# Kernel optimization log

Measured on AMD Instinct MI355X. Metric: run time of the kernel, lower is better.

## Reference

```python
import jax, jax.numpy as jnp
import numpy as np

N_CHARS, EMB, HID = 256, 512, 2048
HIN = EMB + HID  # concat(input_embedding, hidden)
SEQ_LEN = 4096


def setup_inputs() -> dict:
    key = jax.random.key(0)
    ks = jax.random.split(key, 8)
    w = lambda k, shape: (jax.random.normal(k, shape, jnp.float32) / np.sqrt(shape[-1])).astype(jnp.float32)
    return {
        "input_seq": jax.random.randint(ks[0], (SEQ_LEN,), 0, N_CHARS),
        "emb": jax.random.normal(ks[1], (N_CHARS, EMB), jnp.float32) * 0.02,
        "Wf": w(ks[2], (HID, HIN)), "bf": jnp.zeros((HID,), jnp.float32),
        "Wi": w(ks[3], (HID, HIN)), "bi": jnp.zeros((HID,), jnp.float32),
        "Wo": w(ks[4], (HID, HIN)), "bo": jnp.zeros((HID,), jnp.float32),
        "Wc": w(ks[5], (HID, HIN)), "bc": jnp.zeros((HID,), jnp.float32),
        "Wout": w(ks[6], (N_CHARS, HID)), "bout": jnp.zeros((N_CHARS,), jnp.float32),
    }


def reference(input_seq, emb, Wf, bf, Wi, bi, Wo, bo, Wc, bc, Wout, bout):
    x = emb[input_seq]  # [T, EMB]
    H = Wf.shape[0]

    def step(carry, xt):
        h, c = carry
        hi = jnp.concatenate([xt, h])               # [EMB+HID]
        f = jax.nn.sigmoid(Wf @ hi + bf)            # forget gate
        i = jax.nn.sigmoid(Wi @ hi + bi)            # input gate
        o = jax.nn.sigmoid(Wo @ hi + bo)            # output gate
        g = jnp.tanh(Wc @ hi + bc)                  # cell candidate
        c_new = f * c + i * g
        h_new = o * jnp.tanh(c_new)
        out = Wout @ h_new + bout                   # [N_CHARS]
        return (h_new, c_new), out

    init = (jnp.zeros((H,), x.dtype), jnp.zeros((H,), x.dtype))
    (h_last, c_last), out_seq = jax.lax.scan(step, init, x)
    return out_seq, h_last, c_last
```

## Files before the change

kernel.cpp:

```cpp
#include <hip/hip_runtime.h>

#define NCU     256
#define TPB     512
#define HID     2048
#define EMBD    512
#define HIN     2560
#define TSTEPS  4096
#define NCH     256

typedef unsigned long long u64;
typedef float f32x4 __attribute__((ext_vector_type(4)));

__device__ __forceinline__ float sig_(float x) { return 1.f / (1.f + __expf(-x)); }
__device__ __forceinline__ float th_(float x)  { float e = __expf(2.f * x); return 1.f - 2.f / (e + 1.f); }

__device__ __forceinline__ u64 ld_slot(const u64* p) {
    return __hip_atomic_load(p, __ATOMIC_RELAXED, __HIP_MEMORY_SCOPE_AGENT);
}

__device__ __forceinline__ float dot4(f32x4 a, f32x4 b) {
    return a.x * b.x + a.y * b.y + a.z * b.z + a.w * b.w;
}

#define PIN(v) asm volatile("" : "+v"(v))

extern "C" __global__ void __launch_bounds__(TPB, 2)
lstm_persist(const int* __restrict__ seq,
             const float* __restrict__ emb,
             const float* __restrict__ Wf, const float* __restrict__ bf,
             const float* __restrict__ Wi, const float* __restrict__ bi,
             const float* __restrict__ Wo, const float* __restrict__ bo,
             const float* __restrict__ Wc, const float* __restrict__ bc,
             const float* __restrict__ Wout, const float* __restrict__ bout,
             float* __restrict__ dout,
             u64* __restrict__ hbuf)
{
    const int b    = blockIdx.x;
    const int tid  = threadIdx.x;
    const int wave = tid >> 6;
    const int lane = tid & 63;
    const int hidx = b * 8 + wave;

    __shared__ float hs[HID];
    __shared__ float wpart[8];

    f32x4 wh[4][8], wx[4][2], wr;
    {
        const float* Wm[4] = { Wf, Wi, Wo, Wc };
        #pragma unroll
        for (int g = 0; g < 4; ++g) {
            const float* base = Wm[g] + (size_t)hidx * HIN;
            #pragma unroll
            for (int j = 0; j < 8; ++j)
                wh[g][j] = *(const f32x4*)(base + EMBD + 4 * lane + 256 * j);
            #pragma unroll
            for (int j = 0; j < 2; ++j)
                wx[g][j] = *(const f32x4*)(base + 4 * lane + 256 * j);
        }
        wr = *(const f32x4*)(Wout + (size_t)b * HID + 4 * tid);
    }
    const float bias0 = bf[hidx], bias1 = bi[hidx], bias2 = bo[hidx], bias3 = bc[hidx];
    const float boutb = bout[b];

    float c = 0.f;
    int ch = seq[0];

    for (int t = 0; t <= TSTEPS; ++t) {
        #pragma unroll
        for (int g = 0; g < 4; ++g) {
            #pragma unroll
            for (int j = 0; j < 8; ++j) PIN(wh[g][j]);
            PIN(wx[g][0]); PIN(wx[g][1]);
        }
        PIN(wr);

        float a0 = bias0, a1 = bias1, a2 = bias2, a3 = bias3;
        if (t < TSTEPS) {
            const float* erow = emb + (size_t)ch * EMBD;
            const f32x4 xv0 = *(const f32x4*)(erow + 4 * lane);
            const f32x4 xv1 = *(const f32x4*)(erow + 4 * lane + 256);
            a0 += dot4(wx[0][0], xv0) + dot4(wx[0][1], xv1);
            a1 += dot4(wx[1][0], xv0) + dot4(wx[1][1], xv1);
            a2 += dot4(wx[2][0], xv0) + dot4(wx[2][1], xv1);
            a3 += dot4(wx[3][0], xv0) + dot4(wx[3][1], xv1);
        }
        const int ch_next = (t + 1 < TSTEPS) ? seq[t + 1] : 0;

        if (t == 0) {
            #pragma unroll
            for (int k = 0; k < 4; ++k) hs[tid + 512 * k] = 0.f;
        } else {
            const u64* src = hbuf + (size_t)(t & 1) * HID;
            const u64* p0 = src + tid;
            const u64* p1 = src + tid + 512;
            const u64* p2 = src + tid + 1024;
            const u64* p3 = src + tid + 1536;
            const unsigned tt = (unsigned)t;
            u64 v0 = ld_slot(p0), v1 = ld_slot(p1), v2 = ld_slot(p2), v3 = ld_slot(p3);
            while (((unsigned)(v0 >> 32) != tt) | ((unsigned)(v1 >> 32) != tt) |
                   ((unsigned)(v2 >> 32) != tt) | ((unsigned)(v3 >> 32) != tt)) {
                __builtin_amdgcn_s_sleep(1);
                v0 = ld_slot(p0); v1 = ld_slot(p1); v2 = ld_slot(p2); v3 = ld_slot(p3);
            }
            hs[tid]        = __uint_as_float((unsigned)v0);
            hs[tid + 512]  = __uint_as_float((unsigned)v1);
            hs[tid + 1024] = __uint_as_float((unsigned)v2);
            hs[tid + 1536] = __uint_as_float((unsigned)v3);
        }
        __syncthreads();

        if (t < TSTEPS) {
            #pragma unroll
            for (int j = 0; j < 8; ++j) {
                const f32x4 hv = *(const f32x4*)&hs[4 * lane + 256 * j];
                a0 += dot4(wh[0][j], hv);
                a1 += dot4(wh[1][j], hv);
                a2 += dot4(wh[2][j], hv);
                a3 += dot4(wh[3][j], hv);
            }
            #pragma unroll
            for (int m = 32; m >= 1; m >>= 1) {
                a0 += __shfl_xor(a0, m, 64);
                a1 += __shfl_xor(a1, m, 64);
                a2 += __shfl_xor(a2, m, 64);
                a3 += __shfl_xor(a3, m, 64);
            }
            const float f = sig_(a0);
            const float i = sig_(a1);
            const float o = sig_(a2);
            const float g = th_(a3);
            c = f * c + i * g;
            const float hn = o * th_(c);
            if (lane == 0) {
                const u64 pk = ((u64)(unsigned)(t + 1) << 32) | (u64)__float_as_uint(hn);
                __hip_atomic_store(hbuf + (size_t)((t + 1) & 1) * HID + hidx, pk,
                                   __ATOMIC_RELAXED, __HIP_MEMORY_SCOPE_AGENT);
                if (t == TSTEPS - 1) {
                    dout[(size_t)TSTEPS * NCH + hidx]       = hn;
                    dout[(size_t)TSTEPS * NCH + HID + hidx] = c;
                }
            }
        }

        if (t > 0) {
            const f32x4 hv = *(const f32x4*)&hs[4 * tid];
            float op = dot4(wr, hv);
            #pragma unroll
            for (int m = 32; m >= 1; m >>= 1) op += __shfl_xor(op, m, 64);
            if (lane == 0) wpart[wave] = op;
        }
        __syncthreads();

        if (tid == 0 && t > 0) {
            float s = wpart[0] + wpart[1] + wpart[2] + wpart[3]
                    + wpart[4] + wpart[5] + wpart[6] + wpart[7];
            dout[(size_t)(t - 1) * NCH + b] = s + boutb;
        }
        ch = ch_next;
    }
}

extern "C" void kernel_launch(void* const* d_in, const int* in_sizes, int n_in,
                              void* d_out, int out_size, void* d_ws, size_t ws_size,
                              hipStream_t stream) {
    const int*   seq  = (const int*)d_in[0];
    const float* emb  = (const float*)d_in[1];
    const float* Wf   = (const float*)d_in[2];
    const float* bf   = (const float*)d_in[3];
    const float* Wi   = (const float*)d_in[4];
    const float* bi   = (const float*)d_in[5];
    const float* Wo   = (const float*)d_in[6];
    const float* bo   = (const float*)d_in[7];
    const float* Wc   = (const float*)d_in[8];
    const float* bc   = (const float*)d_in[9];
    const float* Wout = (const float*)d_in[10];
    const float* bout = (const float*)d_in[11];
    float* dout = (float*)d_out;
    u64*   hbuf = (u64*)d_ws;

    hipMemsetAsync(d_ws, 0, 2 * HID * sizeof(u64), stream);
    hipLaunchKernelGGL(lstm_persist, dim3(NCU), dim3(TPB), 0, stream,
                       seq, emb, Wf, bf, Wi, bi, Wo, bo, Wc, bc, Wout, bout,
                       dout, hbuf);
}
```

Measured before the change: 10.34 ms.

## Halve block size and map two hidden rows per wave using half-waves

Reduces the block from 8 waves to 4, with each half-wave (32 lanes) owning one hidden row, so every thread holds twice as many register-resident weights. Reductions shrink to a 5-step shuffle and the barrier involves fewer waves, cutting the per-step synchronisation and polling traffic. In exchange, register pressure roughly doubles per thread (about 160 f32x4 vectors), which risks spills. Each step also does more serial FMA work per thread, and each thread now polls 8 slots instead of 4.

```diff
diff --git a/kernel.cpp b/kernel.cpp
--- a/kernel.cpp
+++ b/kernel.cpp
@@ -1,7 +1,7 @@
 #include <hip/hip_runtime.h>
 
 #define NCU     256
-#define TPB     512
+#define TPB     256
 #define HID     2048
 #define EMBD    512
 #define HIN     2560
@@ -24,7 +24,7 @@
 
 #define PIN(v) asm volatile("" : "+v"(v))
 
-extern "C" __global__ void __launch_bounds__(TPB, 2)
+extern "C" __global__ void __launch_bounds__(TPB, 1)
 lstm_persist(const int* __restrict__ seq,
              const float* __restrict__ emb,
              const float* __restrict__ Wf, const float* __restrict__ bf,
@@ -39,27 +39,39 @@
     const int tid  = threadIdx.x;
     const int wave = tid >> 6;
     const int lane = tid & 63;
-    const int hidx = b * 8 + wave;
+    const int half = lane >> 5;
+    const int s    = lane & 31;
+    const int R    = b * 8 + 2 * wave + half;
 
     __shared__ float hs[HID];
-    __shared__ float wpart[8];
-
-    f32x4 wh[4][8], wx[4][2], wr;
+    __shared__ float wpart[4];
+
+    f32x4 wh0[16], wh1[16], wh2[16], wh3[16];
+    f32x4 wx0[4],  wx1[4],  wx2[4],  wx3[4];
+    f32x4 wr0, wr1;
     {
-        const float* Wm[4] = { Wf, Wi, Wo, Wc };
-        #pragma unroll
-        for (int g = 0; g < 4; ++g) {
-            const float* base = Wm[g] + (size_t)hidx * HIN;
-            #pragma unroll
-            for (int j = 0; j < 8; ++j)
-                wh[g][j] = *(const f32x4*)(base + EMBD + 4 * lane + 256 * j);
-            #pragma unroll
-            for (int j = 0; j < 2; ++j)
-                wx[g][j] = *(const f32x4*)(base + 4 * lane + 256 * j);
-        }
-        wr = *(const f32x4*)(Wout + (size_t)b * HID + 4 * tid);
+        const float* b0 = Wf + (size_t)R * HIN;
+        const float* b1 = Wi + (size_t)R * HIN;
+        const float* b2 = Wo + (size_t)R * HIN;
+        const float* b3 = Wc + (size_t)R * HIN;
+        #pragma unroll
+        for (int j = 0; j < 16; ++j) {
+            wh0[j] = *(const f32x4*)(b0 + EMBD + 4 * s + 128 * j);
+            wh1[j] = *(const f32x4*)(b1 + EMBD + 4 * s + 128 * j);
+            wh2[j] = *(const f32x4*)(b2 + EMBD + 4 * s + 128 * j);
+            wh3[j] = *(const f32x4*)(b3 + EMBD + 4 * s + 128 * j);
+        }
+        #pragma unroll
+        for (int j = 0; j < 4; ++j) {
+            wx0[j] = *(const f32x4*)(b0 + 4 * s + 128 * j);
+            wx1[j] = *(const f32x4*)(b1 + 4 * s + 128 * j);
+            wx2[j] = *(const f32x4*)(b2 + 4 * s + 128 * j);
+            wx3[j] = *(const f32x4*)(b3 + 4 * s + 128 * j);
+        }
+        wr0 = *(const f32x4*)(Wout + (size_t)b * HID + 8 * tid);
+        wr1 = *(const f32x4*)(Wout + (size_t)b * HID + 8 * tid + 4);
     }
-    const float bias0 = bf[hidx], bias1 = bi[hidx], bias2 = bo[hidx], bias3 = bc[hidx];
+    const float bias0 = bf[R], bias1 = bi[R], bias2 = bo[R], bias3 = bc[R];
     const float boutb = bout[b];
 
     float c = 0.f;
@@ -67,59 +79,71 @@
 
     for (int t = 0; t <= TSTEPS; ++t) {
         #pragma unroll
-        for (int g = 0; g < 4; ++g) {
-            #pragma unroll
-            for (int j = 0; j < 8; ++j) PIN(wh[g][j]);
-            PIN(wx[g][0]); PIN(wx[g][1]);
-        }
-        PIN(wr);
+        for (int j = 0; j < 16; ++j) { PIN(wh0[j]); PIN(wh1[j]); PIN(wh2[j]); PIN(wh3[j]); }
+        #pragma unroll
+        for (int j = 0; j < 4; ++j)  { PIN(wx0[j]); PIN(wx1[j]); PIN(wx2[j]); PIN(wx3[j]); }
+        PIN(wr0); PIN(wr1);
 
         float a0 = bias0, a1 = bias1, a2 = bias2, a3 = bias3;
         if (t < TSTEPS) {
             const float* erow = emb + (size_t)ch * EMBD;
-            const f32x4 xv0 = *(const f32x4*)(erow + 4 * lane);
-            const f32x4 xv1 = *(const f32x4*)(erow + 4 * lane + 256);
-            a0 += dot4(wx[0][0], xv0) + dot4(wx[0][1], xv1);
-            a1 += dot4(wx[1][0], xv0) + dot4(wx[1][1], xv1);
-            a2 += dot4(wx[2][0], xv0) + dot4(wx[2][1], xv1);
-            a3 += dot4(wx[3][0], xv0) + dot4(wx[3][1], xv1);
+            #pragma unroll
+            for (int j = 0; j < 4; ++j) {
+                const f32x4 xv = *(const f32x4*)(erow + 4 * s + 128 * j);
+                a0 += dot4(wx0[j], xv);
+                a1 += dot4(wx1[j], xv);
+                a2 += dot4(wx2[j], xv);
+                a3 += dot4(wx3[j], xv);
+            }
         }
         const int ch_next = (t + 1 < TSTEPS) ? seq[t + 1] : 0;
 
         if (t == 0) {
             #pragma unroll
-            for (int k = 0; k < 4; ++k) hs[tid + 512 * k] = 0.f;
+            for (int k = 0; k < 8; ++k) hs[tid + 256 * k] = 0.f;
         } else {
             const u64* src = hbuf + (size_t)(t & 1) * HID;
-            const u64* p0 = src + tid;
-            const u64* p1 = src + tid + 512;
-            const u64* p2 = src + tid + 1024;
-            const u64* p3 = src + tid + 1536;
             const unsigned tt = (unsigned)t;
-            u64 v0 = ld_slot(p0), v1 = ld_slot(p1), v2 = ld_slot(p2), v3 = ld_slot(p3);
+            u64 v0 = ld_slot(src + tid);
+            u64 v1 = ld_slot(src + tid + 256);
+            u64 v2 = ld_slot(src + tid + 512);
+            u64 v3 = ld_slot(src + tid + 768);
+            u64 v4 = ld_slot(src + tid + 1024);
+            u64 v5 = ld_slot(src + tid + 1280);
+            u64 v6 = ld_slot(src + tid + 1536);
+            u64 v7 = ld_slot(src + tid + 1792);
             while (((unsigned)(v0 >> 32) != tt) | ((unsigned)(v1 >> 32) != tt) |
-                   ((unsigned)(v2 >> 32) != tt) | ((unsigned)(v3 >> 32) != tt)) {
+                   ((unsigned)(v2 >> 32) != tt) | ((unsigned)(v3 >> 32) != tt) |
+                   ((unsigned)(v4 >> 32) != tt) | ((unsigned)(v5 >> 32) != tt) |
+                   ((unsigned)(v6 >> 32) != tt) | ((unsigned)(v7 >> 32) != tt)) {
                 __builtin_amdgcn_s_sleep(1);
-                v0 = ld_slot(p0); v1 = ld_slot(p1); v2 = ld_slot(p2); v3 = ld_slot(p3);
+                v0 = ld_slot(src + tid);        v1 = ld_slot(src + tid + 256);
+                v2 = ld_slot(src + tid + 512);  v3 = ld_slot(src + tid + 768);
+                v4 = ld_slot(src + tid + 1024); v5 = ld_slot(src + tid + 1280);
+                v6 = ld_slot(src + tid + 1536); v7 = ld_slot(src + tid + 1792);
             }
             hs[tid]        = __uint_as_float((unsigned)v0);
-            hs[tid + 512]  = __uint_as_float((unsigned)v1);
-            hs[tid + 1024] = __uint_as_float((unsigned)v2);
-            hs[tid + 1536] = __uint_as_float((unsigned)v3);
+            hs[tid + 256]  = __uint_as_float((unsigned)v1);
+            hs[tid + 512]  = __uint_as_float((unsigned)v2);
+            hs[tid + 768]  = __uint_as_float((unsigned)v3);
+            hs[tid + 1024] = __uint_as_float((unsigned)v4);
+            hs[tid + 1280] = __uint_as_float((unsigned)v5);
+            hs[tid + 1536] = __uint_as_float((unsigned)v6);
+            hs[tid + 1792] = __uint_as_float((unsigned)v7);
         }
         __syncthreads();
 
         if (t < TSTEPS) {
             #pragma unroll
-            for (int j = 0; j < 8; ++j) {
-                const f32x4 hv = *(const f32x4*)&hs[4 * lane + 256 * j];
-                a0 += dot4(wh[0][j], hv);
-                a1 += dot4(wh[1][j], hv);
-                a2 += dot4(wh[2][j], hv);
-                a3 += dot4(wh[3][j], hv);
-            }
-            #pragma unroll
-            for (int m = 32; m >= 1; m >>= 1) {
+            for (int j = 0; j < 16; ++j) {
+                const f32x4 hv = *(const f32x4*)&hs[4 * s + 128 * j];
+                a0 += dot4(wh0[j], hv);
+                a1 += dot4(wh1[j], hv);
+                a2 += dot4(wh2[j], hv);
+                a3 += dot4(wh3[j], hv);
+            }
+            #pragma unroll
+            for (int m = 16; m >= 1; m >>= 1) {
                 a0 += __shfl_xor(a0, m, 64);
                 a1 += __shfl_xor(a1, m, 64);
                 a2 += __shfl_xor(a2, m, 64);
@@ -131,20 +155,21 @@
             const float g = th_(a3);
             c = f * c + i * g;
             const float hn = o * th_(c);
-            if (lane == 0) {
+            if (s == 0) {
                 const u64 pk = ((u64)(unsigned)(t + 1) << 32) | (u64)__float_as_uint(hn);
-                __hip_atomic_store(hbuf + (size_t)((t + 1) & 1) * HID + hidx, pk,
+                __hip_atomic_store(hbuf + (size_t)((t + 1) & 1) * HID + R, pk,
                                    __ATOMIC_RELAXED, __HIP_MEMORY_SCOPE_AGENT);
                 if (t == TSTEPS - 1) {
-                    dout[(size_t)TSTEPS * NCH + hidx]       = hn;
-                    dout[(size_t)TSTEPS * NCH + HID + hidx] = c;
+                    dout[(size_t)TSTEPS * NCH + R]       = hn;
+                    dout[(size_t)TSTEPS * NCH + HID + R] = c;
                 }
             }
         }
 
         if (t > 0) {
-            const f32x4 hv = *(const f32x4*)&hs[4 * tid];
-            float op = dot4(wr, hv);
+            const f32x4 h0 = *(const f32x4*)&hs[8 * tid];
+            const f32x4 h1 = *(const f32x4*)&hs[8 * tid + 4];
+            float op = dot4(wr0, h0) + dot4(wr1, h1);
             #pragma unroll
             for (int m = 32; m >= 1; m >>= 1) op += __shfl_xor(op, m, 64);
             if (lane == 0) wpart[wave] = op;
@@ -152,9 +177,8 @@
         __syncthreads();
 
         if (tid == 0 && t > 0) {
-            float s = wpart[0] + wpart[1] + wpart[2] + wpart[3]
-                    + wpart[4] + wpart[5] + wpart[6] + wpart[7];
-            dout[(size_t)(t - 1) * NCH + b] = s + boutb;
+            dout[(size_t)(t - 1) * NCH + b] =
+                wpart[0] + wpart[1] + wpart[2] + wpart[3] + boutb;
         }
         ch = ch_next;
     }
```

After: 15.60 ms. +50.9%, slower.
